# Kernel optimization log

Hardware: AMD Instinct MI355X
Metric: run time of the kernel (lower is better)

Reference implementation:

```python
import jax, jax.numpy as jnp
import numpy as np

B, N, C, E, K, L = 8, 20000, 256, 320000, 3, 2
EPS = 1e-5

def setup_inputs() -> dict:
    key = jax.random.key(0)
    ks = jax.random.split(key, 8)
    features = jax.random.normal(ks[0], (B * N, C), dtype=jnp.float32)
    edge_index = jax.random.randint(ks[1], (2, E), 0, N, dtype=jnp.int64)
    # ChebConv params per layer: K linear weights [C,C] (no per-lin bias) + one bias [C]
    W = jax.random.normal(ks[2], (L, K, C, C), dtype=jnp.float32) * 0.05
    b = jax.random.normal(ks[3], (L, C), dtype=jnp.float32) * 0.05
    # node-mode LayerNorm affine params per layer
    ln_w = jnp.ones((L, C), dtype=jnp.float32)
    ln_b = jnp.zeros((L, C), dtype=jnp.float32)
    return {"features": features, "W": W, "b": b, "ln_w": ln_w, "ln_b": ln_b,
            "edge_index": edge_index, "batch_size": B}


def reference(features, W, b, ln_w, ln_b, edge_index, batch_size):
    n = features.shape[0] // batch_size
    c = features.shape[-1]
    src, dst = edge_index[0], edge_index[1]
    # sym-normalized Laplacian, lambda_max=2: L_hat = 2L/lmax - I = -D^-1/2 A D^-1/2
    deg = jax.ops.segment_sum(jnp.ones_like(src, dtype=features.dtype), src, num_segments=n)
    dis = jnp.where(deg > 0, jax.lax.rsqrt(jnp.where(deg > 0, deg, 1.0)), 0.0)
    norm = -dis[src] * dis[dst]  # [E]
    n_layers, k_order = W.shape[0], W.shape[1]

    def prop(x):  # L_hat @ x via gather-scale-scatter
        return jax.ops.segment_sum(norm[:, None] * x[src], dst, num_segments=n)

    def cheb(x, Wl, bl):
        Tx0 = x
        out = Tx0 @ Wl[0]
        Tx1 = prop(Tx0)
        out = out + Tx1 @ Wl[1]
        for k in range(2, k_order):
            Tx2 = 2.0 * prop(Tx1) - Tx0
            out = out + Tx2 @ Wl[k]
            Tx0, Tx1 = Tx1, Tx2
        return out + bl

    def single(feats):  # [n, c] -> [n, c]
        x = feats
        for i in range(n_layers):
            # NOTE: module passes original features to every layer's conv (faithful)
            x = cheb(feats, W[i], b[i])
            mu = jnp.mean(x, axis=-1, keepdims=True)
            var = jnp.var(x, axis=-1, keepdims=True)
            x = (x - mu) * jax.lax.rsqrt(var + EPS) * ln_w[i] + ln_b[i]
            # dropout p=0.0 -> identity
        return x

    fb = features.reshape(batch_size, n, c)
    return jax.vmap(single)(fb)
```

## Files before the change

kernel.cpp:

```cpp
#include <hip/hip_runtime.h>
#include <stdint.h>

#define BB 8
#define NN 20000
#define CC 256
#define EE 320000
#define KK 3
#define MROWS (BB * NN)
#define ROWU (BB * CC)

__device__ __forceinline__ float bf2f(ushort u) {
    union { uint32_t ui; float f; } v; v.ui = ((uint32_t)u) << 16; return v.f;
}
__device__ __forceinline__ ushort f2bf(float f) {
    union { uint32_t ui; float f; } v; v.f = f;
    uint32_t r = (v.ui + 0x7FFFu + ((v.ui >> 16) & 1u)) >> 16;
    return (ushort)r;
}

typedef __bf16 bf16x8 __attribute__((ext_vector_type(8)));
typedef float  f32x4  __attribute__((ext_vector_type(4)));

__device__ __forceinline__ void gload16(const void* gptr, void* lptr) {
    __builtin_amdgcn_global_load_lds(
        (const __attribute__((address_space(1))) void*)gptr,
        (__attribute__((address_space(3))) void*)lptr, 16, 0, 0);
}

__global__ void detect_k(const int* __restrict__ raw, int* __restrict__ flag) {
    int i = blockIdx.x * 256 + threadIdx.x;
    int v = 0;
    int idx = 2 * i + 1;
    if (i < EE) v = raw[idx];
    unsigned long long m = __ballot(v != 0);
    if ((threadIdx.x & 63) == 0 && m) atomicOr(flag, 1);
}

__global__ void convert_k(const int* __restrict__ raw, const int* __restrict__ flag,
                          int* __restrict__ src, int* __restrict__ dst) {
    int e = blockIdx.x * 256 + threadIdx.x;
    if (e >= EE) return;
    if (*flag == 0) {
        src[e] = raw[2 * e];
        dst[e] = raw[2 * EE + 2 * e];
    } else {
        src[e] = raw[e];
        dst[e] = raw[EE + e];
    }
}

__global__ void count_k(const int* __restrict__ src, const int* __restrict__ dst,
                        int* __restrict__ deg_out, int* __restrict__ cnt_in) {
    int e = blockIdx.x * 256 + threadIdx.x;
    if (e >= EE) return;
    atomicAdd(&deg_out[src[e]], 1);
    atomicAdd(&cnt_in[dst[e]], 1);
}

__global__ void __launch_bounds__(1024) scan_k(const int* __restrict__ cnt_in,
                                               const int* __restrict__ deg_out,
                                               int* __restrict__ row_ptr,
                                               float* __restrict__ dis) {
    __shared__ int wpart[16];
    const int t = threadIdx.x;
    const int lane = t & 63, wid = t >> 6;
    const int base = t * 20;
    int local[20];
    int sum = 0;
#pragma unroll
    for (int i = 0; i < 20; i++) {
        int idx = base + i;
        int v = (idx < NN) ? cnt_in[idx] : 0;
        local[i] = sum;
        sum += v;
    }
    int sc = sum;
#pragma unroll
    for (int off = 1; off < 64; off <<= 1) {
        int u = __shfl_up(sc, off, 64);
        if (lane >= off) sc += u;
    }
    if (lane == 63) wpart[wid] = sc;
    __syncthreads();
    if (wid == 0 && lane < 16) {
        int v = wpart[lane];
#pragma unroll
        for (int off = 1; off < 16; off <<= 1) {
            int u = __shfl_up(v, off, 64);
            if (lane >= off) v += u;
        }
        wpart[lane] = v;
    }
    __syncthreads();
    int wbase = (wid > 0) ? wpart[wid - 1] : 0;
    int tbase = wbase + sc - sum;
#pragma unroll
    for (int i = 0; i < 20; i++) {
        int idx = base + i;
        if (idx < NN) row_ptr[idx] = tbase + local[i];
    }
    if (t == 1023) row_ptr[NN] = tbase + sum;
    for (int i = t; i < NN; i += 1024) {
        int d = deg_out[i];
        dis[i] = (d > 0) ? rsqrtf((float)d) : 0.0f;
    }
}

__global__ void fill_k(const int* __restrict__ src, const int* __restrict__ dst,
                       const int* __restrict__ row_ptr, int* __restrict__ fillc,
                       const float* __restrict__ dis,
                       int* __restrict__ col, float* __restrict__ w) {
    int e = blockIdx.x * 256 + threadIdx.x;
    if (e >= EE) return;
    int s = src[e], d = dst[e];
    int pos = row_ptr[d] + atomicAdd(&fillc[d], 1);
    col[pos] = s;
    w[pos] = -dis[s] * dis[d];
}

__global__ void cvt_k(const float* __restrict__ x, ushort* __restrict__ y) {
    size_t idx = ((size_t)blockIdx.x * 256 + threadIdx.x) * 4;
    int row = (int)(idx >> 8);
    int c = (int)(idx & 255);
    int b = row / NN, n = row - b * NN;
    float4 v = *(const float4*)(x + idx);
    ushort4 o = make_ushort4(f2bf(v.x), f2bf(v.y), f2bf(v.z), f2bf(v.w));
    *(ushort4*)(y + ((size_t)(n * BB + b) * CC + c)) = o;
}

__global__ void wprep_k(const float* __restrict__ W, ushort* __restrict__ wt) {
    int idx = blockIdx.x * 256 + threadIdx.x;
    if (idx >= 256 * 768) return;
    int n = idx / 768, k = idx % 768;
    int sel = k >> 8, kk = k & 255;
    const float* W1 = W + KK * CC * CC;
    float v;
    if (sel == 0)      v = W1[kk * CC + n] - W1[2 * CC * CC + kk * CC + n];
    else if (sel == 1) v = W1[CC * CC + kk * CC + n];
    else               v = 2.0f * W1[2 * CC * CC + kk * CC + n];
    wt[idx] = f2bf(v);
}

__global__ void __launch_bounds__(256) prop_k(const ushort* __restrict__ x,
                                              ushort* __restrict__ y,
                                              const int* __restrict__ row_ptr,
                                              const int* __restrict__ col,
                                              const float* __restrict__ w) {
    const int n = blockIdx.x;
    const int t = threadIdx.x;
    const int beg = row_ptr[n], end = row_ptr[n + 1];
    const ushort* xb = x + t * 8;
    float a0 = 0, a1 = 0, a2 = 0, a3 = 0, a4 = 0, a5 = 0, a6 = 0, a7 = 0;
    int j = beg;
    for (; j + 4 <= end; j += 4) {
        int s0 = col[j], s1 = col[j + 1], s2 = col[j + 2], s3 = col[j + 3];
        float w0 = w[j], w1 = w[j + 1], w2 = w[j + 2], w3 = w[j + 3];
        uint4 v0 = *(const uint4*)(xb + (size_t)s0 * ROWU);
        uint4 v1 = *(const uint4*)(xb + (size_t)s1 * ROWU);
        uint4 v2 = *(const uint4*)(xb + (size_t)s2 * ROWU);
        uint4 v3 = *(const uint4*)(xb + (size_t)s3 * ROWU);
        a0 += w0 * bf2f((ushort)v0.x) + w1 * bf2f((ushort)v1.x) + w2 * bf2f((ushort)v2.x) + w3 * bf2f((ushort)v3.x);
        a1 += w0 * bf2f((ushort)(v0.x >> 16)) + w1 * bf2f((ushort)(v1.x >> 16)) + w2 * bf2f((ushort)(v2.x >> 16)) + w3 * bf2f((ushort)(v3.x >> 16));
        a2 += w0 * bf2f((ushort)v0.y) + w1 * bf2f((ushort)v1.y) + w2 * bf2f((ushort)v2.y) + w3 * bf2f((ushort)v3.y);
        a3 += w0 * bf2f((ushort)(v0.y >> 16)) + w1 * bf2f((ushort)(v1.y >> 16)) + w2 * bf2f((ushort)(v2.y >> 16)) + w3 * bf2f((ushort)(v3.y >> 16));
        a4 += w0 * bf2f((ushort)v0.z) + w1 * bf2f((ushort)v1.z) + w2 * bf2f((ushort)v2.z) + w3 * bf2f((ushort)v3.z);
        a5 += w0 * bf2f((ushort)(v0.z >> 16)) + w1 * bf2f((ushort)(v1.z >> 16)) + w2 * bf2f((ushort)(v2.z >> 16)) + w3 * bf2f((ushort)(v3.z >> 16));
        a6 += w0 * bf2f((ushort)v0.w) + w1 * bf2f((ushort)v1.w) + w2 * bf2f((ushort)v2.w) + w3 * bf2f((ushort)v3.w);
        a7 += w0 * bf2f((ushort)(v0.w >> 16)) + w1 * bf2f((ushort)(v1.w >> 16)) + w2 * bf2f((ushort)(v2.w >> 16)) + w3 * bf2f((ushort)(v3.w >> 16));
    }
    for (; j < end; j++) {
        int s = col[j];
        float wt = w[j];
        uint4 v = *(const uint4*)(xb + (size_t)s * ROWU);
        a0 += wt * bf2f((ushort)v.x);
        a1 += wt * bf2f((ushort)(v.x >> 16));
        a2 += wt * bf2f((ushort)v.y);
        a3 += wt * bf2f((ushort)(v.y >> 16));
        a4 += wt * bf2f((ushort)v.z);
        a5 += wt * bf2f((ushort)(v.z >> 16));
        a6 += wt * bf2f((ushort)v.w);
        a7 += wt * bf2f((ushort)(v.w >> 16));
    }
    uint4 o;
    o.x = (uint32_t)f2bf(a0) | ((uint32_t)f2bf(a1) << 16);
    o.y = (uint32_t)f2bf(a2) | ((uint32_t)f2bf(a3) << 16);
    o.z = (uint32_t)f2bf(a4) | ((uint32_t)f2bf(a5) << 16);
    o.w = (uint32_t)f2bf(a6) | ((uint32_t)f2bf(a7) << 16);
    *(uint4*)(y + (size_t)n * ROWU + t * 8) = o;
}

__global__ void __launch_bounds__(256) gemmln_k(const ushort* __restrict__ a0,
                                                const ushort* __restrict__ a1,
                                                const ushort* __restrict__ a2,
                                                const ushort* __restrict__ wt,
                                                const float* __restrict__ bias,
                                                const float* __restrict__ lnw,
                                                const float* __restrict__ lnb,
                                                float* __restrict__ out) {
    __shared__ ushort As[64 * 32];
    __shared__ ushort Bs[256 * 32];
    __shared__ float reds[64][4];
    __shared__ float redq[64][4];
    const int tid = threadIdx.x;
    const int wid = tid >> 6, lane = tid & 63;
    const int quad = lane >> 4, l16 = lane & 15;
    const int row0 = blockIdx.x * 64;

    f32x4 acc[4][4] = {};

    for (int kt = 0; kt < 24; kt++) {
        const ushort* ab = (kt < 8) ? a0 : ((kt < 16) ? a1 : a2);
        const int kl = (kt & 7) * 32;
        const int kg = kt * 32;
        __syncthreads();
        {
            int c = wid * 64 + lane;
            int m = c >> 2, kq = (c & 3) * 8;
            gload16(ab + (size_t)(row0 + m) * CC + kl + kq, &As[(wid * 64) * 8]);
        }
#pragma unroll
        for (int q = 0; q < 4; q++) {
            int c = wid * 256 + q * 64 + lane;
            int m = c >> 2, kq = (c & 3) * 8;
            gload16(wt + (size_t)m * 768 + kg + kq, &Bs[(wid * 256 + q * 64) * 8]);
        }
        __syncthreads();

        bf16x8 af[4], bfr[4];
#pragma unroll
        for (int mt = 0; mt < 4; mt++)
            af[mt] = *(const bf16x8*)&As[(mt * 16 + l16) * 32 + quad * 8];
#pragma unroll
        for (int nt = 0; nt < 4; nt++)
            bfr[nt] = *(const bf16x8*)&Bs[(wid * 64 + nt * 16 + l16) * 32 + quad * 8];
#pragma unroll
        for (int mt = 0; mt < 4; mt++)
#pragma unroll
            for (int nt = 0; nt < 4; nt++)
                acc[mt][nt] = __builtin_amdgcn_mfma_f32_16x16x32_bf16(
                    af[mt], bfr[nt], acc[mt][nt], 0, 0, 0);
    }

    float bv[4], lwv[4], lbv[4];
#pragma unroll
    for (int nt = 0; nt < 4; nt++) {
        int c = wid * 64 + nt * 16 + l16;
        bv[nt] = bias[c]; lwv[nt] = lnw[c]; lbv[nt] = lnb[c];
    }
#pragma unroll
    for (int mt = 0; mt < 4; mt++) {
#pragma unroll
        for (int r = 0; r < 4; r++) {
            float s = 0.0f, q = 0.0f;
#pragma unroll
            for (int nt = 0; nt < 4; nt++) {
                float v = acc[mt][nt][r] + bv[nt];
                s += v; q += v * v;
            }
#pragma unroll
            for (int off = 1; off < 16; off <<= 1) {
                s += __shfl_xor(s, off, 64);
                q += __shfl_xor(q, off, 64);
            }
            if (l16 == 0) {
                int m = mt * 16 + quad * 4 + r;
                reds[m][wid] = s;
                redq[m][wid] = q;
            }
        }
    }
    __syncthreads();
#pragma unroll
    for (int mt = 0; mt < 4; mt++) {
#pragma unroll
        for (int r = 0; r < 4; r++) {
            int ml = mt * 16 + quad * 4 + r;
            float s = reds[ml][0] + reds[ml][1] + reds[ml][2] + reds[ml][3];
            float q = redq[ml][0] + redq[ml][1] + redq[ml][2] + redq[ml][3];
            float mean = s * (1.0f / CC);
            float var = q * (1.0f / CC) - mean * mean;
            float rs = rsqrtf(var + 1e-5f);
            int m = row0 + ml;
            int n = m >> 3, b = m & 7;
            size_t orow = (size_t)b * NN + n;
#pragma unroll
            for (int nt = 0; nt < 4; nt++) {
                int c = wid * 64 + nt * 16 + l16;
                float v = (acc[mt][nt][r] + bv[nt] - mean) * rs * lwv[nt] + lbv[nt];
                out[orow * CC + c] = v;
            }
        }
    }
}

extern "C" void kernel_launch(void* const* d_in, const int* in_sizes, int n_in,
                              void* d_out, int out_size, void* d_ws, size_t ws_size,
                              hipStream_t stream) {
    const float* feats = (const float*)d_in[0];
    const float* W     = (const float*)d_in[1];
    const float* bvec  = (const float*)d_in[2];
    const float* lnw   = (const float*)d_in[3];
    const float* lnb   = (const float*)d_in[4];
    const int*   eidx  = (const int*)d_in[5];
    float* outp = (float*)d_out;

    int* flag    = (int*)d_ws;
    int* deg_out = flag + 64;
    int* cnt_in  = deg_out + NN;
    int* fillc   = cnt_in + NN;
    int* row_ptr = fillc + NN;
    int* srcw    = row_ptr + (NN + 64);
    int* dstw    = srcw + EE;
    int* colw    = dstw + EE;
    float* disw  = (float*)(colw + EE);
    float* ww    = disw + (NN + 64);
    uintptr_t bf_base = ((uintptr_t)(ww + EE) + 255) & ~(uintptr_t)255;
    ushort* featsb = (ushort*)bf_base;
    ushort* tx1b   = featsb + (size_t)MROWS * CC;
    ushort* p2b    = tx1b + (size_t)MROWS * CC;
    ushort* wcat   = p2b + (size_t)MROWS * CC;

    hipMemsetAsync(flag, 0, (size_t)(64 + 3 * NN) * sizeof(int), stream);

    int eb = (EE + 255) / 256;
    detect_k<<<eb, 256, 0, stream>>>(eidx, flag);
    convert_k<<<eb, 256, 0, stream>>>(eidx, flag, srcw, dstw);
    count_k<<<eb, 256, 0, stream>>>(srcw, dstw, deg_out, cnt_in);
    scan_k<<<1, 1024, 0, stream>>>(cnt_in, deg_out, row_ptr, disw);
    fill_k<<<eb, 256, 0, stream>>>(srcw, dstw, row_ptr, fillc, disw, colw, ww);

    cvt_k<<<MROWS * CC / 1024, 256, 0, stream>>>(feats, featsb);
    wprep_k<<<(256 * 768 + 255) / 256, 256, 0, stream>>>(W, wcat);

    prop_k<<<NN, 256, 0, stream>>>(featsb, tx1b, row_ptr, colw, ww);
    prop_k<<<NN, 256, 0, stream>>>(tx1b, p2b, row_ptr, colw, ww);

    gemmln_k<<<MROWS / 64, 256, 0, stream>>>(featsb, tx1b, p2b, wcat,
                                             bvec + CC, lnw + CC, lnb + CC, outp);
}
```

Before: 938.3 us.

## Enlarge GEMM-LN tiles with swizzled LDS and fuse small prep kernels

```diff
diff --git a/kernel.cpp b/kernel.cpp
--- a/kernel.cpp
+++ b/kernel.cpp
@@ -36,25 +36,19 @@
     if ((threadIdx.x & 63) == 0 && m) atomicOr(flag, 1);
 }
 
-__global__ void convert_k(const int* __restrict__ raw, const int* __restrict__ flag,
-                          int* __restrict__ src, int* __restrict__ dst) {
+__global__ void convcount_k(const int* __restrict__ raw, const int* __restrict__ flag,
+                            int mode,
+                            int* __restrict__ src, int* __restrict__ dst,
+                            int* __restrict__ deg_out, int* __restrict__ cnt_in) {
     int e = blockIdx.x * 256 + threadIdx.x;
     if (e >= EE) return;
-    if (*flag == 0) {
-        src[e] = raw[2 * e];
-        dst[e] = raw[2 * EE + 2 * e];
-    } else {
-        src[e] = raw[e];
-        dst[e] = raw[EE + e];
-    }
-}
-
-__global__ void count_k(const int* __restrict__ src, const int* __restrict__ dst,
-                        int* __restrict__ deg_out, int* __restrict__ cnt_in) {
-    int e = blockIdx.x * 256 + threadIdx.x;
-    if (e >= EE) return;
-    atomicAdd(&deg_out[src[e]], 1);
-    atomicAdd(&cnt_in[dst[e]], 1);
+    int m = mode ? mode : (*flag ? 1 : 2);
+    int s, d;
+    if (m == 2) { s = raw[2 * e]; d = raw[2 * EE + 2 * e]; }
+    else        { s = raw[e];     d = raw[EE + e]; }
+    src[e] = s; dst[e] = d;
+    atomicAdd(&deg_out[s], 1);
+    atomicAdd(&cnt_in[d], 1);
 }
 
 __global__ void __launch_bounds__(1024) scan_k(const int* __restrict__ cnt_in,
@@ -118,27 +112,29 @@
     w[pos] = -dis[s] * dis[d];
 }
 
-__global__ void cvt_k(const float* __restrict__ x, ushort* __restrict__ y) {
-    size_t idx = ((size_t)blockIdx.x * 256 + threadIdx.x) * 4;
-    int row = (int)(idx >> 8);
-    int c = (int)(idx & 255);
-    int b = row / NN, n = row - b * NN;
-    float4 v = *(const float4*)(x + idx);
-    ushort4 o = make_ushort4(f2bf(v.x), f2bf(v.y), f2bf(v.z), f2bf(v.w));
-    *(ushort4*)(y + ((size_t)(n * BB + b) * CC + c)) = o;
-}
-
-__global__ void wprep_k(const float* __restrict__ W, ushort* __restrict__ wt) {
-    int idx = blockIdx.x * 256 + threadIdx.x;
-    if (idx >= 256 * 768) return;
-    int n = idx / 768, k = idx % 768;
-    int sel = k >> 8, kk = k & 255;
-    const float* W1 = W + KK * CC * CC;
-    float v;
-    if (sel == 0)      v = W1[kk * CC + n] - W1[2 * CC * CC + kk * CC + n];
-    else if (sel == 1) v = W1[CC * CC + kk * CC + n];
-    else               v = 2.0f * W1[2 * CC * CC + kk * CC + n];
-    wt[idx] = f2bf(v);
+__global__ void cvtwprep_k(const float* __restrict__ x, ushort* __restrict__ y,
+                           const float* __restrict__ W, ushort* __restrict__ wt) {
+    int bid = blockIdx.x;
+    if (bid < MROWS * CC / 1024) {
+        size_t idx = ((size_t)bid * 256 + threadIdx.x) * 4;
+        int row = (int)(idx >> 8);
+        int c = (int)(idx & 255);
+        int b = row / NN, n = row - b * NN;
+        float4 v = *(const float4*)(x + idx);
+        ushort4 o = make_ushort4(f2bf(v.x), f2bf(v.y), f2bf(v.z), f2bf(v.w));
+        *(ushort4*)(y + ((size_t)(n * BB + b) * CC + c)) = o;
+    } else {
+        int idx = (bid - MROWS * CC / 1024) * 256 + threadIdx.x;
+        if (idx >= 256 * 768) return;
+        int n = idx / 768, k = idx % 768;
+        int sel = k >> 8, kk = k & 255;
+        const float* W1 = W + KK * CC * CC;
+        float v;
+        if (sel == 0)      v = W1[kk * CC + n] - W1[2 * CC * CC + kk * CC + n];
+        else if (sel == 1) v = W1[CC * CC + kk * CC + n];
+        else               v = 2.0f * W1[2 * CC * CC + kk * CC + n];
+        wt[idx] = f2bf(v);
+    }
 }
 
 __global__ void __launch_bounds__(256) prop_k(const ushort* __restrict__ x,
@@ -189,62 +185,77 @@
     *(uint4*)(y + (size_t)n * ROWU + t * 8) = o;
 }
 
-__global__ void __launch_bounds__(256) gemmln_k(const ushort* __restrict__ a0,
-                                                const ushort* __restrict__ a1,
-                                                const ushort* __restrict__ a2,
-                                                const ushort* __restrict__ wt,
-                                                const float* __restrict__ bias,
-                                                const float* __restrict__ lnw,
-                                                const float* __restrict__ lnb,
-                                                float* __restrict__ out) {
-    __shared__ ushort As[64 * 32];
-    __shared__ ushort Bs[256 * 32];
-    __shared__ float reds[64][4];
-    __shared__ float redq[64][4];
+__global__ void __launch_bounds__(512, 4) gemmln_k(const ushort* __restrict__ a0,
+                                                   const ushort* __restrict__ a1,
+                                                   const ushort* __restrict__ a2,
+                                                   const ushort* __restrict__ wt,
+                                                   const float* __restrict__ bias,
+                                                   const float* __restrict__ lnw,
+                                                   const float* __restrict__ lnb,
+                                                   float* __restrict__ out) {
+    __shared__ ushort As[128 * 64];
+    __shared__ ushort Bs[256 * 64];
+    __shared__ float reds[128][4];
+    __shared__ float redq[128][4];
     const int tid = threadIdx.x;
     const int wid = tid >> 6, lane = tid & 63;
+    const int wrow = wid >> 2, wcol = wid & 3;
     const int quad = lane >> 4, l16 = lane & 15;
-    const int row0 = blockIdx.x * 64;
+    const int row0 = blockIdx.x * 128;
 
     f32x4 acc[4][4] = {};
 
-    for (int kt = 0; kt < 24; kt++) {
-        const ushort* ab = (kt < 8) ? a0 : ((kt < 16) ? a1 : a2);
-        const int kl = (kt & 7) * 32;
-        const int kg = kt * 32;
+    for (int kt = 0; kt < 12; kt++) {
+        const ushort* ab = (kt < 4) ? a0 : ((kt < 8) ? a1 : a2);
+        const int kl = (kt & 3) * 64;
+        const int kg = kt * 64;
         __syncthreads();
-        {
-            int c = wid * 64 + lane;
-            int m = c >> 2, kq = (c & 3) * 8;
-            gload16(ab + (size_t)(row0 + m) * CC + kl + kq, &As[(wid * 64) * 8]);
-        }
-#pragma unroll
-        for (int q = 0; q < 4; q++) {
-            int c = wid * 256 + q * 64 + lane;
-            int m = c >> 2, kq = (c & 3) * 8;
-            gload16(wt + (size_t)m * 768 + kg + kq, &Bs[(wid * 256 + q * 64) * 8]);
+#pragma unroll
+        for (int q2 = 0; q2 < 2; q2++) {
+            int c = q2 * 512 + tid;
+            int m = c >> 3, p = c & 7;
+            int kq = (p ^ (m & 7)) * 8;
+            gload16(ab + (size_t)(row0 + m) * CC + kl + kq,
+                    &As[(q2 * 512 + wid * 64) * 8]);
+        }
+#pragma unroll
+        for (int q2 = 0; q2 < 4; q2++) {
+            int c = q2 * 512 + tid;
+            int m = c >> 3, p = c & 7;
+            int kq = (p ^ (m & 7)) * 8;
+            gload16(wt + (size_t)m * 768 + kg + kq,
+                    &Bs[(q2 * 512 + wid * 64) * 8]);
         }
         __syncthreads();
 
-        bf16x8 af[4], bfr[4];
-#pragma unroll
-        for (int mt = 0; mt < 4; mt++)
-            af[mt] = *(const bf16x8*)&As[(mt * 16 + l16) * 32 + quad * 8];
-#pragma unroll
-        for (int nt = 0; nt < 4; nt++)
-            bfr[nt] = *(const bf16x8*)&Bs[(wid * 64 + nt * 16 + l16) * 32 + quad * 8];
-#pragma unroll
-        for (int mt = 0; mt < 4; mt++)
-#pragma unroll
-            for (int nt = 0; nt < 4; nt++)
-                acc[mt][nt] = __builtin_amdgcn_mfma_f32_16x16x32_bf16(
-                    af[mt], bfr[nt], acc[mt][nt], 0, 0, 0);
+#pragma unroll
+        for (int ks = 0; ks < 2; ks++) {
+            bf16x8 af[4], bfr[4];
+#pragma unroll
+            for (int mt = 0; mt < 4; mt++) {
+                int r = wrow * 64 + mt * 16 + l16;
+                int pc = (ks * 4 + quad) ^ (r & 7);
+                af[mt] = *(const bf16x8*)&As[r * 64 + pc * 8];
+            }
+#pragma unroll
+            for (int nt = 0; nt < 4; nt++) {
+                int r = wcol * 64 + nt * 16 + l16;
+                int pc = (ks * 4 + quad) ^ (r & 7);
+                bfr[nt] = *(const bf16x8*)&Bs[r * 64 + pc * 8];
+            }
+#pragma unroll
+            for (int mt = 0; mt < 4; mt++)
+#pragma unroll
+                for (int nt = 0; nt < 4; nt++)
+                    acc[mt][nt] = __builtin_amdgcn_mfma_f32_16x16x32_bf16(
+                        af[mt], bfr[nt], acc[mt][nt], 0, 0, 0);
+        }
     }
 
     float bv[4], lwv[4], lbv[4];
 #pragma unroll
     for (int nt = 0; nt < 4; nt++) {
-        int c = wid * 64 + nt * 16 + l16;
+        int c = wcol * 64 + nt * 16 + l16;
         bv[nt] = bias[c]; lwv[nt] = lnw[c]; lbv[nt] = lnb[c];
     }
 #pragma unroll
@@ -263,9 +274,9 @@
                 q += __shfl_xor(q, off, 64);
             }
             if (l16 == 0) {
-                int m = mt * 16 + quad * 4 + r;
-                reds[m][wid] = s;
-                redq[m][wid] = q;
+                int ml = wrow * 64 + mt * 16 + quad * 4 + r;
+                reds[ml][wcol] = s;
+                redq[ml][wcol] = q;
             }
         }
     }
@@ -274,7 +285,7 @@
     for (int mt = 0; mt < 4; mt++) {
 #pragma unroll
         for (int r = 0; r < 4; r++) {
-            int ml = mt * 16 + quad * 4 + r;
+            int ml = wrow * 64 + mt * 16 + quad * 4 + r;
             float s = reds[ml][0] + reds[ml][1] + reds[ml][2] + reds[ml][3];
             float q = redq[ml][0] + redq[ml][1] + redq[ml][2] + redq[ml][3];
             float mean = s * (1.0f / CC);
@@ -285,7 +296,7 @@
             size_t orow = (size_t)b * NN + n;
 #pragma unroll
             for (int nt = 0; nt < 4; nt++) {
-                int c = wid * 64 + nt * 16 + l16;
+                int c = wcol * 64 + nt * 16 + l16;
                 float v = (acc[mt][nt][r] + bv[nt] - mean) * rs * lwv[nt] + lbv[nt];
                 out[orow * CC + c] = v;
             }
@@ -322,19 +333,22 @@
 
     hipMemsetAsync(flag, 0, (size_t)(64 + 3 * NN) * sizeof(int), stream);
 
+    int mode = 0;
+    long long esz = in_sizes ? (long long)in_sizes[5] : 0;
+    if (esz == (long long)2 * EE * 8) mode = 2;
+    else if (esz == (long long)2 * EE * 4) mode = 1;
+
     int eb = (EE + 255) / 256;
-    detect_k<<<eb, 256, 0, stream>>>(eidx, flag);
-    convert_k<<<eb, 256, 0, stream>>>(eidx, flag, srcw, dstw);
-    count_k<<<eb, 256, 0, stream>>>(srcw, dstw, deg_out, cnt_in);
+    if (mode == 0) detect_k<<<eb, 256, 0, stream>>>(eidx, flag);
+    convcount_k<<<eb, 256, 0, stream>>>(eidx, flag, mode, srcw, dstw, deg_out, cnt_in);
     scan_k<<<1, 1024, 0, stream>>>(cnt_in, deg_out, row_ptr, disw);
     fill_k<<<eb, 256, 0, stream>>>(srcw, dstw, row_ptr, fillc, disw, colw, ww);
 
-    cvt_k<<<MROWS * CC / 1024, 256, 0, stream>>>(feats, featsb);
-    wprep_k<<<(256 * 768 + 255) / 256, 256, 0, stream>>>(W, wcat);
+    cvtwprep_k<<<MROWS * CC / 1024 + 768, 256, 0, stream>>>(feats, featsb, W, wcat);
 
     prop_k<<<NN, 256, 0, stream>>>(featsb, tx1b, row_ptr, colw, ww);
     prop_k<<<NN, 256, 0, stream>>>(tx1b, p2b, row_ptr, colw, ww);
 
-    gemmln_k<<<MROWS / 64, 256, 0, stream>>>(featsb, tx1b, p2b, wcat,
-                                             bvec + CC, lnw + CC, lnb + CC, outp);
-}
+    gemmln_k<<<MROWS / 128, 512, 0, stream>>>(featsb, tx1b, p2b, wcat,
+                                              bvec + CC, lnw + CC, lnb + CC, outp);
+}
```

After: 907.5 us. 3.3% less time.
